# Performance work log

Measured on AMD Instinct MI355X. Metric: run time of the kernel, lower is better.

Reference implementation:

```python
import jax, jax.numpy as jnp
import numpy as np

B, T, D, H, UNITS = 32, 2048, 512, 512, 512

def setup_inputs() -> dict:
    key = jax.random.key(0)
    ks = jax.random.split(key, 5)
    scale = 0.02
    return {
        "features": jax.random.normal(ks[0], (B, T, D), dtype=jnp.float32),
        "hidden": jax.random.normal(ks[1], (B, H), dtype=jnp.float32),
        "Wk": jax.random.normal(ks[2], (D, UNITS), dtype=jnp.float32) * scale,
        "Wb": jnp.zeros((UNITS,), dtype=jnp.float32),
        "Uk": jax.random.normal(ks[3], (H, UNITS), dtype=jnp.float32) * scale,
        "Ub": jnp.zeros((UNITS,), dtype=jnp.float32),
        "Vk": jax.random.normal(ks[4], (UNITS, 1), dtype=jnp.float32) * scale,
        "Vb": jnp.zeros((1,), dtype=jnp.float32),
    }

def reference(features, hidden, Wk, Wb, Uk, Ub, Vk, Vb):
    # features: [B, T, D], hidden: [B, H]
    wf = jnp.einsum('btd,du->btu', features, Wk) + Wb          # [B, T, U]
    uh = (hidden @ Uk + Ub)[:, None, :]                        # [B, 1, U]
    score = jnp.tanh(wf + uh)                                  # [B, T, U]
    logits = jnp.einsum('btu,uo->bto', score, Vk) + Vb         # [B, T, 1]
    attention_weights = jax.nn.softmax(logits, axis=1)         # [B, T, 1]
    context_vector = jnp.sum(attention_weights * features, axis=1)  # [B, D]
    return context_vector, attention_weights
```

## Files before the change

kernel.cpp:

```cpp
#include <hip/hip_runtime.h>
#include <stdint.h>


typedef unsigned short ushort_t;
typedef __attribute__((ext_vector_type(8))) short short8;
typedef __attribute__((ext_vector_type(4))) float f32x4;
typedef __attribute__((ext_vector_type(2))) float float2v;
typedef __attribute__((ext_vector_type(2))) __bf16 bf162v;

#define GLOBAL_AS __attribute__((address_space(1)))
#define LDS_AS    __attribute__((address_space(3)))

__device__ __forceinline__ ushort_t f2bf(float f) {
    uint32_t u = __builtin_bit_cast(uint32_t, f);
    u = (u + 0x7fffu + ((u >> 16) & 1u)) >> 16;
    return (ushort_t)u;
}
__device__ __forceinline__ uint32_t pkbf(float a, float b) {
    bf162v r = __builtin_convertvector((float2v){a, b}, bf162v);
    return __builtin_bit_cast(uint32_t, r);
}

__global__ __launch_bounds__(256) void prep_all(
    const float* __restrict__ hidden, const float* __restrict__ Uk,
    const float* __restrict__ Ub, const float* __restrict__ Wb,
    const float* __restrict__ Wk,
    float* __restrict__ uh, ushort_t* __restrict__ WkT)
{
    const int pb = blockIdx.x;
    if (pb < 256) {
        const int b  = pb >> 3;
        const int u  = (pb & 7) * 64 + (threadIdx.x & 63);
        const int k0 = (threadIdx.x >> 6) * 128;
        const float* hr = hidden + b * 512;
        float acc = 0.f;
        #pragma unroll 8
        for (int k = k0; k < k0 + 128; ++k)
            acc += hr[k] * Uk[k * 512 + u];
        __shared__ float red[256];
        red[threadIdx.x] = acc;
        __syncthreads();
        if (threadIdx.x < 64) {
            const int ul = threadIdx.x;
            uh[b * 512 + u] = red[ul] + red[ul + 64] + red[ul + 128] + red[ul + 192]
                            + Ub[u] + Wb[u];
        }
    } else {
        __shared__ float t[32][33];
        const int blk = pb - 256;
        const int ti = blk >> 4;
        const int tj = blk & 15;
        const int tx = threadIdx.x & 31;
        const int ty = threadIdx.x >> 5;
        #pragma unroll
        for (int q = 0; q < 4; ++q) {
            const int r = ty * 4 + q;
            t[r][tx] = Wk[(ti * 32 + r) * 512 + tj * 32 + tx];
        }
        __syncthreads();
        #pragma unroll
        for (int q = 0; q < 4; ++q) {
            const int r = ty * 4 + q;
            WkT[(tj * 32 + r) * 512 + ti * 32 + tx] = f2bf(t[tx][r]);
        }
    }
}

#define APAD 40
__global__ __launch_bounds__(1024, 4) void attn_gemm(
    const float* __restrict__ feats, const ushort_t* __restrict__ WkT,
    const float* __restrict__ uh, const float* __restrict__ Vk,
    float* __restrict__ lg)
{
    __shared__ __align__(16) short As[2][128 * APAD];
    __shared__ __align__(16) short Bs[2][512 * 32];
    __shared__ float uh_s[512];
    __shared__ float vk_s[512];
    __shared__ float lpart[8][128];

    const int tid  = threadIdx.x;
    const int lane = tid & 63;
    const int quad = lane >> 4;
    const int lc   = lane & 15;
    const int wave = tid >> 6;
    const int wm   = wave >> 3;
    const int wn   = wave & 7;
    const int m0   = blockIdx.x * 128;
    const int bidx = m0 >> 11;

    if (tid < 512) {
        uh_s[tid] = uh[bidx * 512 + tid];
        vk_s[tid] = Vk[tid];
    }

    const int rowA = tid >> 3;
    const int kAo  = (tid & 7) * 4;
    const int rB0  = tid >> 2;
    const int sB   = tid & 3;

    f32x4 acc[4][4];
    #pragma unroll
    for (int tm = 0; tm < 4; ++tm)
        #pragma unroll
        for (int tn = 0; tn < 4; ++tn)
            acc[tm][tn] = (f32x4){0.f, 0.f, 0.f, 0.f};

    {
        #pragma unroll
        for (int rnd = 0; rnd < 2; ++rnd) {
            const int li = rnd * 1024 + tid;
            const int rB = rnd * 256 + rB0;
            const int kq = (sB ^ ((rB >> 1) & 3)) * 8;
            const ushort_t* gb = WkT + (size_t)rB * 512 + kq;
            __builtin_amdgcn_global_load_lds(
                (const GLOBAL_AS void*)gb, (LDS_AS void*)(Bs[0] + li * 8), 16, 0, 0);
        }
        const f32x4 av = *(const f32x4*)(feats + (size_t)(m0 + rowA) * 512 + kAo);
        uint2 w;
        w.x = pkbf(av.x, av.y);
        w.y = pkbf(av.z, av.w);
        *(uint2*)(As[0] + rowA * APAD + kAo) = w;
    }

    const int swzR = (lc >> 1) & 3;

    int buf = 0;
    for (int ks = 0; ks < 16; ++ks) {
        __syncthreads();

        f32x4 a_next;
        const bool have = (ks + 1) < 16;
        if (have) {
            const int k0n = (ks + 1) * 32;
            #pragma unroll
            for (int rnd = 0; rnd < 2; ++rnd) {
                const int li = rnd * 1024 + tid;
                const int rB = rnd * 256 + rB0;
                const int kq = (sB ^ ((rB >> 1) & 3)) * 8;
                const ushort_t* gb = WkT + (size_t)rB * 512 + k0n + kq;
                __builtin_amdgcn_global_load_lds(
                    (const GLOBAL_AS void*)gb, (LDS_AS void*)(Bs[buf ^ 1] + li * 8),
                    16, 0, 0);
            }
            a_next = *(const f32x4*)(feats + (size_t)(m0 + rowA) * 512 + k0n + kAo);
        }

        short8 af[4], bfr[4];
        #pragma unroll
        for (int t4 = 0; t4 < 4; ++t4) {
            af[t4]  = *(const short8*)(As[buf] + (wm * 64 + t4 * 16 + lc) * APAD + quad * 8);
            bfr[t4] = *(const short8*)(Bs[buf] + (wn * 64 + t4 * 16 + lc) * 32
                                       + ((quad ^ swzR) * 8));
        }
        #pragma unroll
        for (int tm = 0; tm < 4; ++tm)
            #pragma unroll
            for (int tn = 0; tn < 4; ++tn)
                acc[tm][tn] = __builtin_amdgcn_mfma_f32_16x16x32_bf16(
                    af[tm], bfr[tn], acc[tm][tn], 0, 0, 0);

        if (have) {
            uint2 w;
            w.x = pkbf(a_next.x, a_next.y);
            w.y = pkbf(a_next.z, a_next.w);
            *(uint2*)(As[buf ^ 1] + rowA * APAD + kAo) = w;
        }
        buf ^= 1;
    }

    float rp[16];
    #pragma unroll
    for (int i = 0; i < 16; ++i) rp[i] = 0.f;
    #pragma unroll
    for (int tn = 0; tn < 4; ++tn) {
        const int nl  = wn * 64 + tn * 16 + lc;
        const float uhv = uh_s[nl];
        const float vkv = vk_s[nl];
        #pragma unroll
        for (int tm = 0; tm < 4; ++tm)
            #pragma unroll
            for (int i = 0; i < 4; ++i) {
                const float x = acc[tm][tn][i] + uhv;
                const float e = __expf(2.0f * x);
                rp[tm * 4 + i] += (1.0f - 2.0f / (e + 1.0f)) * vkv;
            }
    }
    #pragma unroll
    for (int i = 0; i < 16; ++i) {
        float v = rp[i];
        v += __shfl_xor(v, 1, 64);
        v += __shfl_xor(v, 2, 64);
        v += __shfl_xor(v, 4, 64);
        v += __shfl_xor(v, 8, 64);
        rp[i] = v;
    }
    if (lc == 0) {
        #pragma unroll
        for (int tm = 0; tm < 4; ++tm)
            #pragma unroll
            for (int i = 0; i < 4; ++i)
                lpart[wn][wm * 64 + tm * 16 + quad * 4 + i] = rp[tm * 4 + i];
    }
    __syncthreads();
    if (tid < 128) {
        float s = 0.f;
        #pragma unroll
        for (int j = 0; j < 8; ++j) s += lpart[j][tid];
        lg[m0 + tid] = s;
    }
}

__global__ __launch_bounds__(256) void softmax_k(
    const float* __restrict__ lg, float* __restrict__ aw_out)
{
    const int b = blockIdx.x, tid = threadIdx.x;
    const float* p = lg + b * 2048;
    float v[8];
    #pragma unroll
    for (int i = 0; i < 8; ++i) v[i] = p[tid + i * 256];
    float mx = -1e30f;
    #pragma unroll
    for (int i = 0; i < 8; ++i) mx = fmaxf(mx, v[i]);
    #pragma unroll
    for (int off = 32; off >= 1; off >>= 1) mx = fmaxf(mx, __shfl_xor(mx, off, 64));
    __shared__ float redm[4], reds[4];
    const int wv = tid >> 6, ln = tid & 63;
    if (ln == 0) redm[wv] = mx;
    __syncthreads();
    mx = fmaxf(fmaxf(redm[0], redm[1]), fmaxf(redm[2], redm[3]));
    float s = 0.f;
    #pragma unroll
    for (int i = 0; i < 8; ++i) { v[i] = __expf(v[i] - mx); s += v[i]; }
    #pragma unroll
    for (int off = 32; off >= 1; off >>= 1) s += __shfl_xor(s, off, 64);
    if (ln == 0) reds[wv] = s;
    __syncthreads();
    s = reds[0] + reds[1] + reds[2] + reds[3];
    const float inv = 1.0f / s;
    #pragma unroll
    for (int i = 0; i < 8; ++i)
        aw_out[b * 2048 + tid + i * 256] = v[i] * inv;
}

__global__ __launch_bounds__(256) void context_part(
    const float* __restrict__ feats, const float* __restrict__ aw,
    float* __restrict__ part)
{
    const int b     = blockIdx.x >> 4;
    const int chunk = blockIdx.x & 15;
    const int half  = threadIdx.x >> 7;
    const int t0    = chunk * 128 + half * 64;
    const int d4    = (threadIdx.x & 127) * 4;
    const float* wp = aw + b * 2048 + t0;
    const float* fp = feats + (size_t)(b * 2048 + t0) * 512 + d4;
    f32x4 a = (f32x4){0.f, 0.f, 0.f, 0.f};
    #pragma unroll 4
    for (int tt = 0; tt < 64; ++tt) {
        const float w = wp[tt];
        const f32x4 f = *(const f32x4*)(fp + (size_t)tt * 512);
        a.x += w * f.x; a.y += w * f.y; a.z += w * f.z; a.w += w * f.w;
    }
    *(f32x4*)(part + (size_t)(b * 32 + chunk * 2 + half) * 512 + d4) = a;
}

__global__ __launch_bounds__(512) void context_reduce(
    const float* __restrict__ part, float* __restrict__ ctx)
{
    const int b = blockIdx.x;
    const int d = threadIdx.x;
    const float* p = part + (size_t)b * 32 * 512 + d;
    float s = 0.f;
    #pragma unroll
    for (int j = 0; j < 32; ++j) s += p[j * 512];
    ctx[b * 512 + d] = s;
}

extern "C" void kernel_launch(void* const* d_in, const int* in_sizes, int n_in,
                              void* d_out, int out_size, void* d_ws, size_t ws_size,
                              hipStream_t stream)
{
    const float* feats  = (const float*)d_in[0];
    const float* hidden = (const float*)d_in[1];
    const float* Wk     = (const float*)d_in[2];
    const float* Wb     = (const float*)d_in[3];
    const float* Uk     = (const float*)d_in[4];
    const float* Ub     = (const float*)d_in[5];
    const float* Vk     = (const float*)d_in[6];

    float* out       = (float*)d_out;
    float* ctx_out_p = out;
    float* aw_out_p  = out + 16384;

    char* ws = (char*)d_ws;
    float*    uh   = (float*)ws;
    ushort_t* WkT  = (ushort_t*)(ws + 65536);
    float*    lg   = (float*)(ws + 589824);
    float*    part = (float*)(ws + 851968);

    prep_all      <<<512, 256, 0, stream>>>(hidden, Uk, Ub, Wb, Wk, uh, WkT);
    attn_gemm     <<<512, 1024, 0, stream>>>(feats, WkT, uh, Vk, lg);
    softmax_k     <<<32,  256, 0, stream>>>(lg, aw_out_p);
    context_part  <<<512, 256, 0, stream>>>(feats, aw_out_p, part);
    context_reduce<<<32,  512, 0, stream>>>(part, ctx_out_p);
}
```

Measured before the change: 257.4 us.

## Pre-swizzle Wk into MFMA fragment order and read B directly from global

The prep kernel now writes Wk as bf16 in the exact per-lane MFMA fragment layout, so the GEMM kernel loads B operands straight from global memory (cached in L2) instead of staging them through LDS. The GEMM tile shrinks to 64 rows with 512 threads and 8 waves each covering 64 columns, doubling the grid. This removes the LDS traffic and buffer space for B, which may raise occupancy. In exchange, B is re-read from global/L2 by every block without LDS reuse, and the global loads sit on the MFMA critical path without prefetching.

```diff
diff --git a/kernel.cpp b/kernel.cpp
--- a/kernel.cpp
+++ b/kernel.cpp
@@ -8,9 +8,6 @@
 typedef __attribute__((ext_vector_type(2))) float float2v;
 typedef __attribute__((ext_vector_type(2))) __bf16 bf162v;
 
-#define GLOBAL_AS __attribute__((address_space(1)))
-#define LDS_AS    __attribute__((address_space(3)))
-
 __device__ __forceinline__ ushort_t f2bf(float f) {
     uint32_t u = __builtin_bit_cast(uint32_t, f);
     u = (u + 0x7fffu + ((u >> 16) & 1u)) >> 16;
@@ -25,7 +22,7 @@
     const float* __restrict__ hidden, const float* __restrict__ Uk,
     const float* __restrict__ Ub, const float* __restrict__ Wb,
     const float* __restrict__ Wk,
-    float* __restrict__ uh, ushort_t* __restrict__ WkT)
+    float* __restrict__ uh, ushort_t* __restrict__ WkTf)
 {
     const int pb = blockIdx.x;
     if (pb < 256) {
@@ -46,57 +43,60 @@
                             + Ub[u] + Wb[u];
         }
     } else {
-        __shared__ float t[32][33];
-        const int blk = pb - 256;
-        const int ti = blk >> 4;
-        const int tj = blk & 15;
-        const int tx = threadIdx.x & 31;
-        const int ty = threadIdx.x >> 5;
-        #pragma unroll
-        for (int q = 0; q < 4; ++q) {
-            const int r = ty * 4 + q;
-            t[r][tx] = Wk[(ti * 32 + r) * 512 + tj * 32 + tx];
+        __shared__ float t[32][17];
+        const int tid = threadIdx.x;
+        #pragma unroll
+        for (int e = 0; e < 2; ++e) {
+            const int g  = (pb - 256) * 2 + e;
+            const int ks = g >> 5;
+            const int n4 = g & 31;
+            #pragma unroll
+            for (int q = 0; q < 2; ++q) {
+                const int idx = q * 256 + tid;
+                const int dl  = idx >> 4;
+                const int ul  = idx & 15;
+                t[dl][ul] = Wk[(size_t)(ks * 32 + dl) * 512 + n4 * 16 + ul];
+            }
+            __syncthreads();
+            #pragma unroll
+            for (int q = 0; q < 2; ++q) {
+                const int idx  = q * 256 + tid;
+                const int j    = idx & 7;
+                const int lc   = (idx >> 3) & 15;
+                const int quad = idx >> 7;
+                WkTf[(size_t)g * 512 + idx] = f2bf(t[quad * 8 + j][lc]);
+            }
+            __syncthreads();
         }
-        __syncthreads();
-        #pragma unroll
-        for (int q = 0; q < 4; ++q) {
-            const int r = ty * 4 + q;
-            WkT[(tj * 32 + r) * 512 + ti * 32 + tx] = f2bf(t[tx][r]);
-        }
     }
 }
 
 #define APAD 40
-__global__ __launch_bounds__(1024, 4) void attn_gemm(
-    const float* __restrict__ feats, const ushort_t* __restrict__ WkT,
+__global__ __launch_bounds__(512, 4) void attn_gemm(
+    const float* __restrict__ feats, const ushort_t* __restrict__ WkTf,
     const float* __restrict__ uh, const float* __restrict__ Vk,
     float* __restrict__ lg)
 {
-    __shared__ __align__(16) short As[2][128 * APAD];
-    __shared__ __align__(16) short Bs[2][512 * 32];
+    __shared__ __align__(16) short As[2][64 * APAD];
     __shared__ float uh_s[512];
     __shared__ float vk_s[512];
-    __shared__ float lpart[8][128];
+    __shared__ float lpart[8][64];
 
     const int tid  = threadIdx.x;
     const int lane = tid & 63;
     const int quad = lane >> 4;
     const int lc   = lane & 15;
-    const int wave = tid >> 6;
-    const int wm   = wave >> 3;
-    const int wn   = wave & 7;
-    const int m0   = blockIdx.x * 128;
+    const int wn   = tid >> 6;
+    const int m0   = blockIdx.x * 64;
     const int bidx = m0 >> 11;
 
-    if (tid < 512) {
-        uh_s[tid] = uh[bidx * 512 + tid];
-        vk_s[tid] = Vk[tid];
-    }
+    uh_s[tid] = uh[bidx * 512 + tid];
+    vk_s[tid] = Vk[tid];
 
     const int rowA = tid >> 3;
     const int kAo  = (tid & 7) * 4;
-    const int rB0  = tid >> 2;
-    const int sB   = tid & 3;
+
+    const ushort_t* bbase = WkTf + (size_t)(wn * 4) * 512 + quad * 128 + lc * 8;
 
     f32x4 acc[4][4];
     #pragma unroll
@@ -106,15 +106,6 @@
             acc[tm][tn] = (f32x4){0.f, 0.f, 0.f, 0.f};
 
     {
-        #pragma unroll
-        for (int rnd = 0; rnd < 2; ++rnd) {
-            const int li = rnd * 1024 + tid;
-            const int rB = rnd * 256 + rB0;
-            const int kq = (sB ^ ((rB >> 1) & 3)) * 8;
-            const ushort_t* gb = WkT + (size_t)rB * 512 + kq;
-            __builtin_amdgcn_global_load_lds(
-                (const GLOBAL_AS void*)gb, (LDS_AS void*)(Bs[0] + li * 8), 16, 0, 0);
-        }
         const f32x4 av = *(const f32x4*)(feats + (size_t)(m0 + rowA) * 512 + kAo);
         uint2 w;
         w.x = pkbf(av.x, av.y);
@@ -122,36 +113,25 @@
         *(uint2*)(As[0] + rowA * APAD + kAo) = w;
     }
 
-    const int swzR = (lc >> 1) & 3;
-
     int buf = 0;
     for (int ks = 0; ks < 16; ++ks) {
         __syncthreads();
 
         f32x4 a_next;
         const bool have = (ks + 1) < 16;
-        if (have) {
-            const int k0n = (ks + 1) * 32;
-            #pragma unroll
-            for (int rnd = 0; rnd < 2; ++rnd) {
-                const int li = rnd * 1024 + tid;
-                const int rB = rnd * 256 + rB0;
-                const int kq = (sB ^ ((rB >> 1) & 3)) * 8;
-                const ushort_t* gb = WkT + (size_t)rB * 512 + k0n + kq;
-                __builtin_amdgcn_global_load_lds(
-                    (const GLOBAL_AS void*)gb, (LDS_AS void*)(Bs[buf ^ 1] + li * 8),
-                    16, 0, 0);
-            }
-            a_next = *(const f32x4*)(feats + (size_t)(m0 + rowA) * 512 + k0n + kAo);
-        }
+        if (have)
+            a_next = *(const f32x4*)(feats + (size_t)(m0 + rowA) * 512
+                                     + (ks + 1) * 32 + kAo);
 
         short8 af[4], bfr[4];
-        #pragma unroll
-        for (int t4 = 0; t4 < 4; ++t4) {
-            af[t4]  = *(const short8*)(As[buf] + (wm * 64 + t4 * 16 + lc) * APAD + quad * 8);
-            bfr[t4] = *(const short8*)(Bs[buf] + (wn * 64 + t4 * 16 + lc) * 32
-                                       + ((quad ^ swzR) * 8));
-        }
+        const ushort_t* bk = bbase + (size_t)ks * 16384;
+        #pragma unroll
+        for (int t4 = 0; t4 < 4; ++t4)
+            bfr[t4] = *(const short8*)(bk + t4 * 512);
+        #pragma unroll
+        for (int t4 = 0; t4 < 4; ++t4)
+            af[t4] = *(const short8*)(As[buf] + (t4 * 16 + lc) * APAD + quad * 8);
+
         #pragma unroll
         for (int tm = 0; tm < 4; ++tm)
             #pragma unroll
@@ -199,10 +179,10 @@
         for (int tm = 0; tm < 4; ++tm)
             #pragma unroll
             for (int i = 0; i < 4; ++i)
-                lpart[wn][wm * 64 + tm * 16 + quad * 4 + i] = rp[tm * 4 + i];
+                lpart[wn][tm * 16 + quad * 4 + i] = rp[tm * 4 + i];
     }
     __syncthreads();
-    if (tid < 128) {
+    if (tid < 64) {
         float s = 0.f;
         #pragma unroll
         for (int j = 0; j < 8; ++j) s += lpart[j][tid];
@@ -293,12 +273,12 @@
 
     char* ws = (char*)d_ws;
     float*    uh   = (float*)ws;
-    ushort_t* WkT  = (ushort_t*)(ws + 65536);
+    ushort_t* WkTf = (ushort_t*)(ws + 65536);
     float*    lg   = (float*)(ws + 589824);
     float*    part = (float*)(ws + 851968);
 
-    prep_all      <<<512, 256, 0, stream>>>(hidden, Uk, Ub, Wb, Wk, uh, WkT);
-    attn_gemm     <<<512, 1024, 0, stream>>>(feats, WkT, uh, Vk, lg);
+    prep_all      <<<512, 256, 0, stream>>>(hidden, Uk, Ub, Wb, Wk, uh, WkTf);
+    attn_gemm     <<<1024, 512, 0, stream>>>(feats, WkTf, uh, Vk, lg);
     softmax_k     <<<32,  256, 0, stream>>>(lg, aw_out_p);
     context_part  <<<512, 256, 0, stream>>>(feats, aw_out_p, part);
     context_reduce<<<32,  512, 0, stream>>>(part, ctx_out_p);
```

After: 265.7 us. +3.2%, slower.

## Split attention GEMM over N into 128x128 tiles with XCD-aware block mapping

Applied to the files above, without the earlier changes.

The fused GEMM+tanh+dot kernel moves from 512 blocks of 1024 threads, each covering all 512 output units, to 2048 blocks of 256 threads, each covering a 128x128 tile. Block indices are remapped so consecutive work lands on the same XCD, which should let the four N-tiles of one row block share the feature rows in L2. Partial logits per N-tile are written out and summed inside the softmax kernel. The intent is higher occupancy and better scheduling with smaller blocks. The cost is that each feature row is loaded and converted to bf16 four times, and the partial-logit buffer needs more workspace.

```diff
diff --git a/kernel.cpp b/kernel.cpp
--- a/kernel.cpp
+++ b/kernel.cpp
@@ -5,6 +5,7 @@
 typedef unsigned short ushort_t;
 typedef __attribute__((ext_vector_type(8))) short short8;
 typedef __attribute__((ext_vector_type(4))) float f32x4;
+typedef __attribute__((ext_vector_type(4))) uint32_t u32x4;
 typedef __attribute__((ext_vector_type(2))) float float2v;
 typedef __attribute__((ext_vector_type(2))) __bf16 bf162v;
 
@@ -67,34 +68,39 @@
 }
 
 #define APAD 40
-__global__ __launch_bounds__(1024, 4) void attn_gemm(
+__global__ __launch_bounds__(256, 4) void attn_gemm(
     const float* __restrict__ feats, const ushort_t* __restrict__ WkT,
     const float* __restrict__ uh, const float* __restrict__ Vk,
-    float* __restrict__ lg)
+    float* __restrict__ lgp)
 {
     __shared__ __align__(16) short As[2][128 * APAD];
-    __shared__ __align__(16) short Bs[2][512 * 32];
-    __shared__ float uh_s[512];
-    __shared__ float vk_s[512];
-    __shared__ float lpart[8][128];
+    __shared__ __align__(16) short Bs[2][128 * 32];
+    __shared__ float uh_s[128];
+    __shared__ float vk_s[128];
+    __shared__ float lpart[2][128];
 
     const int tid  = threadIdx.x;
     const int lane = tid & 63;
     const int quad = lane >> 4;
     const int lc   = lane & 15;
     const int wave = tid >> 6;
-    const int wm   = wave >> 3;
-    const int wn   = wave & 7;
-    const int m0   = blockIdx.x * 128;
+    const int wm   = wave >> 1;
+    const int wn   = wave & 1;
+
+    const int wg = (blockIdx.x & 7) * 256 + (blockIdx.x >> 3);
+    const int mt = wg >> 2;
+    const int nt = wg & 3;
+    const int m0 = mt * 128;
+    const int n0 = nt * 128;
     const int bidx = m0 >> 11;
 
-    if (tid < 512) {
-        uh_s[tid] = uh[bidx * 512 + tid];
-        vk_s[tid] = Vk[tid];
-    }
-
-    const int rowA = tid >> 3;
-    const int kAo  = (tid & 7) * 4;
+    if (tid < 128) {
+        uh_s[tid] = uh[bidx * 512 + n0 + tid];
+        vk_s[tid] = Vk[n0 + tid];
+    }
+
+    const int rowA = tid >> 1;
+    const int kh   = (tid & 1) * 16;
     const int rB0  = tid >> 2;
     const int sB   = tid & 3;
 
@@ -108,18 +114,24 @@
     {
         #pragma unroll
         for (int rnd = 0; rnd < 2; ++rnd) {
-            const int li = rnd * 1024 + tid;
-            const int rB = rnd * 256 + rB0;
+            const int li = rnd * 256 + tid;
+            const int rB = rnd * 64 + rB0;
             const int kq = (sB ^ ((rB >> 1) & 3)) * 8;
-            const ushort_t* gb = WkT + (size_t)rB * 512 + kq;
+            const ushort_t* gb = WkT + (size_t)(n0 + rB) * 512 + kq;
             __builtin_amdgcn_global_load_lds(
                 (const GLOBAL_AS void*)gb, (LDS_AS void*)(Bs[0] + li * 8), 16, 0, 0);
         }
-        const f32x4 av = *(const f32x4*)(feats + (size_t)(m0 + rowA) * 512 + kAo);
-        uint2 w;
-        w.x = pkbf(av.x, av.y);
-        w.y = pkbf(av.z, av.w);
-        *(uint2*)(As[0] + rowA * APAD + kAo) = w;
+        const float* ap = feats + (size_t)(m0 + rowA) * 512 + kh;
+        const f32x4 a0 = *(const f32x4*)(ap);
+        const f32x4 a1 = *(const f32x4*)(ap + 4);
+        const f32x4 a2 = *(const f32x4*)(ap + 8);
+        const f32x4 a3 = *(const f32x4*)(ap + 12);
+        u32x4 w0 = (u32x4){pkbf(a0.x,a0.y), pkbf(a0.z,a0.w),
+                           pkbf(a1.x,a1.y), pkbf(a1.z,a1.w)};
+        u32x4 w1 = (u32x4){pkbf(a2.x,a2.y), pkbf(a2.z,a2.w),
+                           pkbf(a3.x,a3.y), pkbf(a3.z,a3.w)};
+        *(u32x4*)(As[0] + rowA * APAD + kh)     = w0;
+        *(u32x4*)(As[0] + rowA * APAD + kh + 8) = w1;
     }
 
     const int swzR = (lc >> 1) & 3;
@@ -128,21 +140,25 @@
     for (int ks = 0; ks < 16; ++ks) {
         __syncthreads();
 
-        f32x4 a_next;
+        f32x4 a0n, a1n, a2n, a3n;
         const bool have = (ks + 1) < 16;
         if (have) {
             const int k0n = (ks + 1) * 32;
             #pragma unroll
             for (int rnd = 0; rnd < 2; ++rnd) {
-                const int li = rnd * 1024 + tid;
-                const int rB = rnd * 256 + rB0;
+                const int li = rnd * 256 + tid;
+                const int rB = rnd * 64 + rB0;
                 const int kq = (sB ^ ((rB >> 1) & 3)) * 8;
-                const ushort_t* gb = WkT + (size_t)rB * 512 + k0n + kq;
+                const ushort_t* gb = WkT + (size_t)(n0 + rB) * 512 + k0n + kq;
                 __builtin_amdgcn_global_load_lds(
                     (const GLOBAL_AS void*)gb, (LDS_AS void*)(Bs[buf ^ 1] + li * 8),
                     16, 0, 0);
             }
-            a_next = *(const f32x4*)(feats + (size_t)(m0 + rowA) * 512 + k0n + kAo);
+            const float* ap = feats + (size_t)(m0 + rowA) * 512 + k0n + kh;
+            a0n = *(const f32x4*)(ap);
+            a1n = *(const f32x4*)(ap + 4);
+            a2n = *(const f32x4*)(ap + 8);
+            a3n = *(const f32x4*)(ap + 12);
         }
 
         short8 af[4], bfr[4];
@@ -160,10 +176,12 @@
                     af[tm], bfr[tn], acc[tm][tn], 0, 0, 0);
 
         if (have) {
-            uint2 w;
-            w.x = pkbf(a_next.x, a_next.y);
-            w.y = pkbf(a_next.z, a_next.w);
-            *(uint2*)(As[buf ^ 1] + rowA * APAD + kAo) = w;
+            u32x4 w0 = (u32x4){pkbf(a0n.x,a0n.y), pkbf(a0n.z,a0n.w),
+                               pkbf(a1n.x,a1n.y), pkbf(a1n.z,a1n.w)};
+            u32x4 w1 = (u32x4){pkbf(a2n.x,a2n.y), pkbf(a2n.z,a2n.w),
+                               pkbf(a3n.x,a3n.y), pkbf(a3n.z,a3n.w)};
+            *(u32x4*)(As[buf ^ 1] + rowA * APAD + kh)     = w0;
+            *(u32x4*)(As[buf ^ 1] + rowA * APAD + kh + 8) = w1;
         }
         buf ^= 1;
     }
@@ -202,22 +220,22 @@
                 lpart[wn][wm * 64 + tm * 16 + quad * 4 + i] = rp[tm * 4 + i];
     }
     __syncthreads();
-    if (tid < 128) {
-        float s = 0.f;
-        #pragma unroll
-        for (int j = 0; j < 8; ++j) s += lpart[j][tid];
-        lg[m0 + tid] = s;
-    }
+    if (tid < 128)
+        lgp[(size_t)(mt * 4 + nt) * 128 + tid] = lpart[0][tid] + lpart[1][tid];
 }
 
 __global__ __launch_bounds__(256) void softmax_k(
-    const float* __restrict__ lg, float* __restrict__ aw_out)
+    const float* __restrict__ lgp, float* __restrict__ aw_out)
 {
     const int b = blockIdx.x, tid = threadIdx.x;
-    const float* p = lg + b * 2048;
     float v[8];
     #pragma unroll
-    for (int i = 0; i < 8; ++i) v[i] = p[tid + i * 256];
+    for (int i = 0; i < 8; ++i) {
+        const int m  = b * 2048 + tid + i * 256;
+        const int mt = m >> 7, row = m & 127;
+        const float* q = lgp + (size_t)mt * 4 * 128 + row;
+        v[i] = q[0] + q[128] + q[256] + q[384];
+    }
     float mx = -1e30f;
     #pragma unroll
     for (int i = 0; i < 8; ++i) mx = fmaxf(mx, v[i]);
@@ -294,12 +312,12 @@
     char* ws = (char*)d_ws;
     float*    uh   = (float*)ws;
     ushort_t* WkT  = (ushort_t*)(ws + 65536);
-    float*    lg   = (float*)(ws + 589824);
-    float*    part = (float*)(ws + 851968);
+    float*    lgp  = (float*)(ws + 589824);
+    float*    part = (float*)(ws + 1638400);
 
     prep_all      <<<512, 256, 0, stream>>>(hidden, Uk, Ub, Wb, Wk, uh, WkT);
-    attn_gemm     <<<512, 1024, 0, stream>>>(feats, WkT, uh, Vk, lg);
-    softmax_k     <<<32,  256, 0, stream>>>(lg, aw_out_p);
+    attn_gemm     <<<2048, 256, 0, stream>>>(feats, WkT, uh, Vk, lgp);
+    softmax_k     <<<32,  256, 0, stream>>>(lgp, aw_out_p);
     context_part  <<<512, 256, 0, stream>>>(feats, aw_out_p, part);
     context_reduce<<<32,  512, 0, stream>>>(part, ctx_out_p);
 }
```

New measurement: 286.0 us. 11.1% more time.

## Fuse softmax into context partial kernel and widen the context split

Applied to the files above, without the earlier changes.

Drops the standalone softmax kernel. Each of 2048 context blocks now recomputes the per-batch max and sum from the logits and derives its weights on the fly, and only chunk 0 writes the attention weights. The time split goes from 32 to 128 partials per batch, with a matching reduce kernel launched as more, smaller blocks. This saves one launch and the dependency on a 32-block softmax pass, at the cost of redundant logit reads per block and a partial buffer four times larger to write and reduce.

```diff
diff --git a/kernel.cpp b/kernel.cpp
--- a/kernel.cpp
+++ b/kernel.cpp
@@ -210,11 +210,15 @@
     }
 }
 
-__global__ __launch_bounds__(256) void softmax_k(
-    const float* __restrict__ lg, float* __restrict__ aw_out)
-{
-    const int b = blockIdx.x, tid = threadIdx.x;
-    const float* p = lg + b * 2048;
+__global__ __launch_bounds__(256) void softmax_ctx(
+    const float* __restrict__ lg, const float* __restrict__ feats,
+    float* __restrict__ aw_out, float* __restrict__ part)
+{
+    const int b     = blockIdx.x >> 6;
+    const int chunk = blockIdx.x & 63;
+    const int tid   = threadIdx.x;
+    const float* p  = lg + b * 2048;
+
     float v[8];
     #pragma unroll
     for (int i = 0; i < 8; ++i) v[i] = p[tid + i * 256];
@@ -237,41 +241,37 @@
     __syncthreads();
     s = reds[0] + reds[1] + reds[2] + reds[3];
     const float inv = 1.0f / s;
-    #pragma unroll
-    for (int i = 0; i < 8; ++i)
-        aw_out[b * 2048 + tid + i * 256] = v[i] * inv;
-}
-
-__global__ __launch_bounds__(256) void context_part(
-    const float* __restrict__ feats, const float* __restrict__ aw,
-    float* __restrict__ part)
-{
-    const int b     = blockIdx.x >> 4;
-    const int chunk = blockIdx.x & 15;
-    const int half  = threadIdx.x >> 7;
-    const int t0    = chunk * 128 + half * 64;
-    const int d4    = (threadIdx.x & 127) * 4;
-    const float* wp = aw + b * 2048 + t0;
+
+    if (chunk == 0) {
+        #pragma unroll
+        for (int i = 0; i < 8; ++i)
+            aw_out[b * 2048 + tid + i * 256] = v[i] * inv;
+    }
+
+    const int half = tid >> 7;
+    const int t0   = chunk * 32 + half * 16;
+    const int d4   = (tid & 127) * 4;
+    const float* wp = lg + b * 2048 + t0;
     const float* fp = feats + (size_t)(b * 2048 + t0) * 512 + d4;
     f32x4 a = (f32x4){0.f, 0.f, 0.f, 0.f};
     #pragma unroll 4
-    for (int tt = 0; tt < 64; ++tt) {
-        const float w = wp[tt];
+    for (int tt = 0; tt < 16; ++tt) {
+        const float w = __expf(wp[tt] - mx) * inv;
         const f32x4 f = *(const f32x4*)(fp + (size_t)tt * 512);
         a.x += w * f.x; a.y += w * f.y; a.z += w * f.z; a.w += w * f.w;
     }
-    *(f32x4*)(part + (size_t)(b * 32 + chunk * 2 + half) * 512 + d4) = a;
-}
-
-__global__ __launch_bounds__(512) void context_reduce(
+    *(f32x4*)(part + (size_t)((b * 64 + chunk) * 2 + half) * 512 + d4) = a;
+}
+
+__global__ __launch_bounds__(64) void context_reduce(
     const float* __restrict__ part, float* __restrict__ ctx)
 {
-    const int b = blockIdx.x;
-    const int d = threadIdx.x;
-    const float* p = part + (size_t)b * 32 * 512 + d;
+    const int b = blockIdx.x >> 3;
+    const int d = (blockIdx.x & 7) * 64 + threadIdx.x;
+    const float* p = part + (size_t)b * 128 * 512 + d;
     float s = 0.f;
-    #pragma unroll
-    for (int j = 0; j < 32; ++j) s += p[j * 512];
+    #pragma unroll 8
+    for (int j = 0; j < 128; ++j) s += p[j * 512];
     ctx[b * 512 + d] = s;
 }
 
@@ -299,7 +299,6 @@
 
     prep_all      <<<512, 256, 0, stream>>>(hidden, Uk, Ub, Wb, Wk, uh, WkT);
     attn_gemm     <<<512, 1024, 0, stream>>>(feats, WkT, uh, Vk, lg);
-    softmax_k     <<<32,  256, 0, stream>>>(lg, aw_out_p);
-    context_part  <<<512, 256, 0, stream>>>(feats, aw_out_p, part);
-    context_reduce<<<32,  512, 0, stream>>>(part, ctx_out_p);
-}
+    softmax_ctx   <<<2048, 256, 0, stream>>>(lg, feats, aw_out_p, part);
+    context_reduce<<<256, 64, 0, stream>>>(part, ctx_out_p);
+}
```

After: 263.8 us. 1.02x slower.
